# Kernel tuning notes

Hardware: AMD Instinct MI355X
Metric: run time of the kernel (lower is better)

## Reference

```python
import jax, jax.numpy as jnp
import numpy as np

EMBED_DIM = 1024
NUM_HEADS = 16
HEAD_DIM = EMBED_DIM // NUM_HEADS


def setup_inputs() -> dict:
    key = jax.random.key(0)
    ks = jax.random.split(key, 10)
    s = 1.0 / np.sqrt(EMBED_DIM)
    inp = {
        "x1": jax.random.normal(ks[0], (4, 1024, EMBED_DIM), jnp.float32),
        "x2": jax.random.normal(ks[1], (4, 2048, EMBED_DIM), jnp.float32),
        "Wq": jax.random.normal(ks[2], (EMBED_DIM, EMBED_DIM), jnp.float32) * s,
        "bq": jnp.zeros((EMBED_DIM,), jnp.float32),
        "Wk": jax.random.normal(ks[3], (EMBED_DIM, EMBED_DIM), jnp.float32) * s,
        "bk": jnp.zeros((EMBED_DIM,), jnp.float32),
        "Wv": jax.random.normal(ks[4], (EMBED_DIM, EMBED_DIM), jnp.float32) * s,
        "bv": jnp.zeros((EMBED_DIM,), jnp.float32),
        "Wo": jax.random.normal(ks[5], (EMBED_DIM, EMBED_DIM), jnp.float32) * s,
        "bo": jnp.zeros((EMBED_DIM,), jnp.float32),
    }
    return inp


def reference(x1, x2, Wq, bq, Wk, bk, Wv, bv, Wo, bo):
    B, Sq, E = x1.shape
    Skv = x2.shape[1]
    H, D = NUM_HEADS, HEAD_DIM
    # linear projections (PyTorch Linear: x @ W.T + b)
    q = (x1 @ Wq.T + bq).reshape(B, Sq, H, D).transpose(0, 2, 1, 3)   # [B,H,Sq,D]
    k = (x2 @ Wk.T + bk).reshape(B, Skv, H, D).transpose(0, 2, 1, 3)  # [B,H,Skv,D]
    v = (x2 @ Wv.T + bv).reshape(B, Skv, H, D).transpose(0, 2, 1, 3)
    scores = jnp.einsum("bhqd,bhkd->bhqk", q, k) / jnp.sqrt(jnp.float32(D))
    attn = jax.nn.softmax(scores, axis=-1)
    out = jnp.einsum("bhqk,bhkd->bhqd", attn, v)
    out = out.transpose(0, 2, 1, 3).reshape(B, Sq, E)
    return out @ Wo.T + bo
```

## Files before the change

kernel.cpp:

```cpp
#include <hip/hip_runtime.h>

typedef __attribute__((ext_vector_type(8))) short short8;
typedef __attribute__((ext_vector_type(4))) short short4v;
typedef __attribute__((ext_vector_type(4))) float f32x4;
typedef _Float16 half8 __attribute__((ext_vector_type(8)));

#define ASYNC16(g, l) __builtin_amdgcn_global_load_lds( \
    (__attribute__((address_space(1))) void*)(g), \
    (__attribute__((address_space(3))) void*)(l), 16, 0, 0)

__device__ __forceinline__ short f2bf(float f) {
  union { float f; unsigned u; } v; v.f = f;
  unsigned r = v.u + 0x7fffu + ((v.u >> 16) & 1u);
  return (short)(r >> 16);
}

__device__ __forceinline__ short f2h(float f) {
  _Float16 h = (_Float16)f;
  return __builtin_bit_cast(short, h);
}

__device__ __forceinline__ unsigned pkh2(float a, float b) {
  return __builtin_bit_cast(unsigned, __builtin_amdgcn_cvt_pkrtz(a, b));
}

__device__ __forceinline__ f32x4 fzero4() {
  f32x4 z; z[0] = 0.f; z[1] = 0.f; z[2] = 0.f; z[3] = 0.f; return z;
}

__device__ __forceinline__ void wg_barrier() {
  asm volatile("s_waitcnt lgkmcnt(0)\n\ts_barrier" ::: "memory");
}

__device__ __forceinline__ void wait4_barrier() {
  asm volatile("s_waitcnt vmcnt(4)\n\ts_barrier" ::: "memory");
}
__device__ __forceinline__ void wait6_barrier() {
  asm volatile("s_waitcnt vmcnt(6)\n\ts_barrier" ::: "memory");
}
__device__ __forceinline__ void wait0_barrier() {
  asm volatile("s_waitcnt vmcnt(0)\n\ts_barrier" ::: "memory");
}

__global__ __launch_bounds__(256) void cvt_all(
    const float* __restrict__ x1, const float* __restrict__ x2,
    const float* __restrict__ wq, const float* __restrict__ wk,
    const float* __restrict__ wv, const float* __restrict__ wo,
    short* __restrict__ dst) {
  long e = ((long)blockIdx.x * 256 + threadIdx.x) * 4;
  const float* src; long loc;
  if (e < 4194304L)       { src = x1; loc = e; }
  else if (e < 12582912L) { src = x2; loc = e - 4194304L; }
  else if (e < 13631488L) { src = wq; loc = e - 12582912L; }
  else if (e < 14680064L) { src = wk; loc = e - 13631488L; }
  else if (e < 15728640L) { src = wv; loc = e - 14680064L; }
  else                    { src = wo; loc = e - 15728640L; }
  float4 v = *(const float4*)(src + loc);
  short4v o;
  o[0] = f2bf(v.x); o[1] = f2bf(v.y); o[2] = f2bf(v.z); o[3] = f2bf(v.w);
  *(short4v*)(dst + e) = o;
}

__global__ __launch_bounds__(256) void proj(
    const short* __restrict__ xb1, const short* __restrict__ xb2,
    const short* __restrict__ wqp, const short* __restrict__ wkp, const short* __restrict__ wvp,
    const float* __restrict__ bq, const float* __restrict__ bk, const float* __restrict__ bv,
    short* __restrict__ qb, short* __restrict__ kb, short* __restrict__ vb) {
  __shared__ short smem[16384];
  const int tid = threadIdx.x, w = tid >> 6, lane = tid & 63;
  const int quad = lane >> 4, col = lane & 15;
  const int waveM = (w >> 1) * 64, waveN = (w & 1) * 64;
  const int my = blockIdx.x, bn = blockIdx.y * 128;
  const short* A; const short* W; const float* bias; int mode, bm;
  if (my < 32)      { A = xb1; W = wqp; bias = bq; mode = 0; bm = my * 128; }
  else if (my < 96) { A = xb2; W = wkp; bias = bk; mode = 1; bm = (my - 32) * 128; }
  else              { A = xb2; W = wvp; bias = bv; mode = 2; bm = (my - 96) * 128; }

  f32x4 acc[4][4];
  for (int mi = 0; mi < 4; ++mi)
    for (int ni = 0; ni < 4; ++ni)
      acc[mi][ni] = fzero4();

  const int srow = w * 16 + (lane >> 2), scol = (lane & 3) * 8;
  const short* ga = A + (size_t)(bm + srow) * 1024 + scol;
  const short* gb = W + (size_t)(bn + srow) * 1024 + scol;

  auto stage = [&](int b, int kk) {
    short* lA = smem + b * 8192 + w * 512;
    short* lB = smem + b * 8192 + 4096 + w * 512;
    ASYNC16(ga + kk,         lA);
    ASYNC16(ga + kk + 65536, lA + 2048);
    ASYNC16(gb + kk,         lB);
    ASYNC16(gb + kk + 65536, lB + 2048);
  };
  auto compute = [&](int b) {
    const short* As_ = smem + b * 8192;
    const short* Bs_ = As_ + 4096;
    short8 af[4], bf[4];
    for (int mi = 0; mi < 4; ++mi)
      af[mi] = *(const short8*)(As_ + (waveM + mi * 16 + col) * 32 + quad * 8);
    for (int ni = 0; ni < 4; ++ni)
      bf[ni] = *(const short8*)(Bs_ + (waveN + ni * 16 + col) * 32 + quad * 8);
    for (int mi = 0; mi < 4; ++mi)
      for (int ni = 0; ni < 4; ++ni)
        acc[mi][ni] = __builtin_amdgcn_mfma_f32_16x16x32_bf16(af[mi], bf[ni], acc[mi][ni], 0, 0, 0);
  };

  stage(0, 0);
  stage(1, 32);
  for (int it = 0; it < 30; ++it) {
    wait4_barrier();
    compute(it & 1);
    wg_barrier();
    stage(it & 1, (it + 2) * 32);
  }
  wait4_barrier();
  compute(0);
  wait0_barrier();
  compute(1);

  for (int ni = 0; ni < 4; ++ni) {
    int nn = waveN + ni * 16 + col;
    float bvl = bias[bn + nn];
    for (int mi = 0; mi < 4; ++mi) {
      int m0 = waveM + mi * 16 + quad * 4;
      for (int r = 0; r < 4; ++r) {
        int m = m0 + r;
        float val = acc[mi][ni][r] + bvl;
        short sv;
        if (mode == 0)      sv = f2bf(val * 0.18033688011112042f);
        else if (mode == 1) sv = f2bf(val);
        else                sv = f2h(val);
        smem[m * 128 + (nn ^ ((m & 15) << 3))] = sv;
      }
    }
  }
  __syncthreads();
  if (mode < 2) {
    const int S = (mode == 0) ? 1024 : 2048;
    short* outp = (mode == 0) ? qb : kb;
    const int bb = bm / S, s0 = bm & (S - 1), h0 = bn >> 6;
    for (int it = 0; it < 8; ++it) {
      int f = (it * 256 + tid) * 8;
      int hh = f >> 13, rem = f & 8191, m = rem >> 6, d = rem & 63;
      int nn = hh * 64 + d;
      short8 val = *(const short8*)&smem[m * 128 + (nn ^ ((m & 15) << 3))];
      *(short8*)(outp + ((((size_t)(bb * 16 + h0 + hh)) * S + s0 + m) * 64 + d)) = val;
    }
  } else {
    const int bb = bm >> 11, s0 = bm & 2047, kt0 = s0 >> 6, h0 = bn >> 6;
    for (int it = 0; it < 8; ++it) {
      int f = (it * 256 + tid) * 8;
      int hh = f >> 13, rem = f & 8191, ktl = rem >> 12, r3 = rem & 4095;
      int d = r3 >> 6, kvp0 = r3 & 63;
      int nn = hh * 64 + d;
      short8 val;
      for (int j = 0; j < 8; ++j) {
        int kvp = kvp0 + j;
        int kv = ((kvp & 3) << 4) | (kvp >> 2);
        int m = ktl * 64 + kv;
        val[j] = smem[m * 128 + (nn ^ ((m & 15) << 3))];
      }
      *(short8*)(vb + ((((size_t)(bb * 16 + h0 + hh)) * 32 + (kt0 + ktl)) * 4096) + d * 64 + kvp0) = val;
    }
  }
}

__global__ __launch_bounds__(256) void out_gemm(
    const short* __restrict__ A, const short* __restrict__ W,
    const float* __restrict__ bias, float* __restrict__ out) {
  __shared__ short smem[24576];
  const int tid = threadIdx.x, w = tid >> 6, lane = tid & 63;
  const int quad = lane >> 4, col = lane & 15;
  const int waveM = (w >> 1) * 64, waveN = (w & 1) * 32;
  const int bn = blockIdx.x * 64, bm = blockIdx.y * 128;

  f32x4 acc[4][2];
  for (int mi = 0; mi < 4; ++mi)
    for (int ni = 0; ni < 2; ++ni)
      acc[mi][ni] = fzero4();

  const int arow = w * 16 + (lane >> 2), ac = (lane & 3) * 8;
  const short* ga = A + (size_t)(bm + arow) * 1024 + ac;
  const short* gb = W + (size_t)(bn + (tid >> 2)) * 1024 + (tid & 3) * 8;

  auto stage = [&](int b, int kk) {
    short* base = smem + b * 12288;
    short* lA0 = base + w * 512;
    short* lA1 = base + 4096 + w * 512;
    short* lB0 = base + 8192 + w * 512;
    short* lB1 = base + 10240 + w * 512;
    ASYNC16(ga + kk,              lA0);
    ASYNC16(ga + kk + 65536,      lA0 + 2048);
    ASYNC16(ga + kk + 32,         lA1);
    ASYNC16(ga + kk + 32 + 65536, lA1 + 2048);
    ASYNC16(gb + kk,              lB0);
    ASYNC16(gb + kk + 32,         lB1);
  };
  auto compute = [&](int b) {
    const short* base = smem + b * 12288;
    for (int kh = 0; kh < 2; ++kh) {
      const short* Ash = base + kh * 4096;
      const short* Bsh = base + 8192 + kh * 2048;
      short8 af[4], bf[2];
      for (int mi = 0; mi < 4; ++mi)
        af[mi] = *(const short8*)(Ash + (waveM + mi * 16 + col) * 32 + quad * 8);
      for (int ni = 0; ni < 2; ++ni)
        bf[ni] = *(const short8*)(Bsh + (waveN + ni * 16 + col) * 32 + quad * 8);
      for (int mi = 0; mi < 4; ++mi)
        for (int ni = 0; ni < 2; ++ni)
          acc[mi][ni] = __builtin_amdgcn_mfma_f32_16x16x32_bf16(af[mi], bf[ni], acc[mi][ni], 0, 0, 0);
    }
  };

  stage(0, 0);
  stage(1, 64);
  for (int it = 0; it < 14; ++it) {
    wait6_barrier();
    compute(it & 1);
    wg_barrier();
    stage(it & 1, (it + 2) * 64);
  }
  wait6_barrier();
  compute(0);
  wait0_barrier();
  compute(1);

  for (int ni = 0; ni < 2; ++ni) {
    int n = bn + waveN + ni * 16 + col;
    float bvl = bias[n];
    for (int mi = 0; mi < 4; ++mi) {
      int m0 = bm + waveM + mi * 16 + quad * 4;
      for (int r = 0; r < 4; ++r)
        out[(size_t)(m0 + r) * 1024 + n] = acc[mi][ni][r] + bvl;
    }
  }
}

__global__ __launch_bounds__(256, 2) void attn(
    const short* __restrict__ Q, const short* __restrict__ K,
    const short* __restrict__ V, short* __restrict__ O) {
  __shared__ short Ks[128 * 72];
  __shared__ short Vs[80 * 136];
  __shared__ short Ps[128 * 136];
  const int tid = threadIdx.x, w = tid >> 6, lane = tid & 63;
  const int quad = lane >> 4, col = lane & 15;
  const int bh = blockIdx.x, qt = blockIdx.y;
  const int b = bh >> 4, h = bh & 15;
  const int qbase = w * 32;

  const short* qp = Q + ((size_t)bh * 1024 + qt * 128) * 64;
  const short* kp = K + (size_t)bh * 131072;
  const short* vp = V + (size_t)bh * 131072;

  short8 aq[2][2];
  for (int mi = 0; mi < 2; ++mi) {
    const short* qr = qp + (qbase + mi * 16 + col) * 64 + quad * 8;
    aq[mi][0] = *(const short8*)qr;
    aq[mi][1] = *(const short8*)(qr + 32);
  }

  f32x4 oa[2][5];
  for (int mi = 0; mi < 2; ++mi)
    for (int ni = 0; ni < 5; ++ni)
      oa[mi][ni] = fzero4();

  for (int i = tid; i < 16 * 136; i += 256)
    Vs[64 * 136 + i] = (i < 136) ? (short)0x3C00 : (short)0;

  const int krow = lane + (w >> 1) * 64, kch = (w & 1) * 32;
  const int vd = lane, vch = w & 1, vkh = (w >> 1) * 32;

  short8 kpre[4], vpre[4];
  {
    const short* kg = kp + krow * 64 + kch;
    const short* vg = vp + vch * 4096 + vd * 64 + vkh;
    for (int i = 0; i < 4; ++i) kpre[i] = *(const short8*)(kg + i * 8);
    for (int i = 0; i < 4; ++i) vpre[i] = *(const short8*)(vg + i * 8);
  }

  for (int kt = 0; kt < 16; ++kt) {
    wg_barrier();
    for (int i = 0; i < 4; ++i)
      *(short8*)&Ks[krow * 72 + kch + i * 8] = kpre[i];
    for (int i = 0; i < 4; ++i)
      *(short8*)&Vs[vd * 136 + vch * 64 + vkh + i * 8] = vpre[i];
    {
      int ktn = (kt < 15) ? kt + 1 : kt;
      const short* kg = kp + ktn * 8192 + krow * 64 + kch;
      const short* vg = vp + (2 * ktn + vch) * 4096 + vd * 64 + vkh;
      for (int i = 0; i < 4; ++i) kpre[i] = *(const short8*)(kg + i * 8);
      for (int i = 0; i < 4; ++i) vpre[i] = *(const short8*)(vg + i * 8);
    }
    wg_barrier();

    f32x4 sf[2][8];
    for (int nk = 0; nk < 8; ++nk) {
      short8 bk0 = *(const short8*)&Ks[(nk * 16 + col) * 72 + quad * 8];
      short8 bk1 = *(const short8*)&Ks[(nk * 16 + col) * 72 + 32 + quad * 8];
      f32x4 z0 = fzero4(), z1 = fzero4();
      z0 = __builtin_amdgcn_mfma_f32_16x16x32_bf16(aq[0][0], bk0, z0, 0, 0, 0);
      z0 = __builtin_amdgcn_mfma_f32_16x16x32_bf16(aq[0][1], bk1, z0, 0, 0, 0);
      z1 = __builtin_amdgcn_mfma_f32_16x16x32_bf16(aq[1][0], bk0, z1, 0, 0, 0);
      z1 = __builtin_amdgcn_mfma_f32_16x16x32_bf16(aq[1][1], bk1, z1, 0, 0, 0);
      sf[0][nk] = z0;
      sf[1][nk] = z1;
    }

    for (int mi = 0; mi < 2; ++mi)
      for (int nk = 0; nk < 8; ++nk)
        for (int r = 0; r < 4; ++r)
          sf[mi][nk][r] = __builtin_amdgcn_exp2f(sf[mi][nk][r]);
    for (int mi = 0; mi < 2; ++mi)
      for (int r = 0; r < 4; ++r) {
        int row = qbase + mi * 16 + quad * 4 + r;
        uint2 d0, d1;
        d0.x = pkh2(sf[mi][0][r], sf[mi][1][r]);
        d0.y = pkh2(sf[mi][2][r], sf[mi][3][r]);
        d1.x = pkh2(sf[mi][4][r], sf[mi][5][r]);
        d1.y = pkh2(sf[mi][6][r], sf[mi][7][r]);
        *(uint2*)&Ps[row * 136 + col * 4]      = d0;
        *(uint2*)&Ps[row * 136 + 64 + col * 4] = d1;
      }

    for (int ks = 0; ks < 4; ++ks) {
      int koff = ks * 32 + quad * 8;
      half8 ap0 = *(const half8*)&Ps[(qbase + col) * 136 + koff];
      half8 ap1 = *(const half8*)&Ps[(qbase + 16 + col) * 136 + koff];
      for (int ni = 0; ni < 5; ++ni) {
        half8 bv = *(const half8*)&Vs[(ni * 16 + col) * 136 + koff];
        oa[0][ni] = __builtin_amdgcn_mfma_f32_16x16x32_f16(ap0, bv, oa[0][ni], 0, 0, 0);
        oa[1][ni] = __builtin_amdgcn_mfma_f32_16x16x32_f16(ap1, bv, oa[1][ni], 0, 0, 0);
      }
    }
  }

  float inv[2][4];
  for (int mi = 0; mi < 2; ++mi)
    for (int r = 0; r < 4; ++r) {
      float s = __shfl(oa[mi][4][r], lane & 48);
      inv[mi][r] = 1.f / s;
    }
  __syncthreads();
  for (int mi = 0; mi < 2; ++mi)
    for (int ni = 0; ni < 4; ++ni)
      for (int r = 0; r < 4; ++r)
        Ps[(qbase + mi * 16 + quad * 4 + r) * 64 + ni * 16 + col] = f2bf(oa[mi][ni][r] * inv[mi][r]);
  __syncthreads();
  for (int it = 0; it < 4; ++it) {
    int f = (it * 256 + tid) * 8;
    int q = f >> 6, d = f & 63;
    short8 val = *(const short8*)&Ps[q * 64 + d];
    *(short8*)(O + ((size_t)(b * 1024 + qt * 128 + q)) * 1024 + h * 64 + d) = val;
  }
}

extern "C" void kernel_launch(void* const* d_in, const int* in_sizes, int n_in,
                              void* d_out, int out_size, void* d_ws, size_t ws_size,
                              hipStream_t stream) {
  const float* x1 = (const float*)d_in[0];
  const float* x2 = (const float*)d_in[1];
  const float* Wq = (const float*)d_in[2];
  const float* bq = (const float*)d_in[3];
  const float* Wk = (const float*)d_in[4];
  const float* bk = (const float*)d_in[5];
  const float* Wv = (const float*)d_in[6];
  const float* bv = (const float*)d_in[7];
  const float* Wo = (const float*)d_in[8];
  const float* bo = (const float*)d_in[9];

  char* ws = (char*)d_ws;
  short* xb1 = (short*)(ws + 0);
  short* xb2 = (short*)(ws + 8388608);
  short* wqb = (short*)(ws + 25165824);
  short* wkb = (short*)(ws + 27262976);
  short* wvb = (short*)(ws + 29360128);
  short* wob = (short*)(ws + 31457280);
  short* qb  = (short*)(ws + 33554432);
  short* kb  = (short*)(ws + 41943040);
  short* vb  = (short*)(ws + 58720256);
  short* ob  = (short*)(ws + 75497472);

  cvt_all<<<16384, 256, 0, stream>>>(x1, x2, Wq, Wk, Wv, Wo, (short*)ws);
  proj<<<dim3(160, 8), 256, 0, stream>>>(xb1, xb2, wqb, wkb, wvb, bq, bk, bv, qb, kb, vb);
  attn<<<dim3(64, 8), 256, 0, stream>>>(qb, kb, vb, ob);
  out_gemm<<<dim3(16, 32), 256, 0, stream>>>(ob, wob, bo, (float*)d_out);
}
```

Baseline: 233.9 us.

## Replace double-buffered projection loop with single-buffer sync loop; add MFMA priority hints

The projection GEMM drops its two-stage async LDS double buffering with vmcnt-based waits and uses a plain single-buffered loop with __syncthreads before and after each stage. Separately, the attention kernel raises wave priority with s_setprio around the QK^T and PV MFMA blocks. The simpler projection loop removes load/compute overlap and exposes global-load latency, while the priority hints aim to favour matrix work when several waves compete for the unit.

```diff
diff --git a/kernel.cpp b/kernel.cpp
--- a/kernel.cpp
+++ b/kernel.cpp
@@ -32,9 +32,6 @@
   asm volatile("s_waitcnt lgkmcnt(0)\n\ts_barrier" ::: "memory");
 }
 
-__device__ __forceinline__ void wait4_barrier() {
-  asm volatile("s_waitcnt vmcnt(4)\n\ts_barrier" ::: "memory");
-}
 __device__ __forceinline__ void wait6_barrier() {
   asm volatile("s_waitcnt vmcnt(6)\n\ts_barrier" ::: "memory");
 }
@@ -67,6 +64,8 @@
     const float* __restrict__ bq, const float* __restrict__ bk, const float* __restrict__ bv,
     short* __restrict__ qb, short* __restrict__ kb, short* __restrict__ vb) {
   __shared__ short smem[16384];
+  short* As = smem;
+  short* Bs = smem + 4096;
   const int tid = threadIdx.x, w = tid >> 6, lane = tid & 63;
   const int quad = lane >> 4, col = lane & 15;
   const int waveM = (w >> 1) * 64, waveN = (w & 1) * 64;
@@ -84,41 +83,27 @@
   const int srow = w * 16 + (lane >> 2), scol = (lane & 3) * 8;
   const short* ga = A + (size_t)(bm + srow) * 1024 + scol;
   const short* gb = W + (size_t)(bn + srow) * 1024 + scol;
-
-  auto stage = [&](int b, int kk) {
-    short* lA = smem + b * 8192 + w * 512;
-    short* lB = smem + b * 8192 + 4096 + w * 512;
+  short* lA = As + w * 512;
+  short* lB = Bs + w * 512;
+
+  for (int kk = 0; kk < 1024; kk += 32) {
+    __syncthreads();
     ASYNC16(ga + kk,         lA);
     ASYNC16(ga + kk + 65536, lA + 2048);
     ASYNC16(gb + kk,         lB);
     ASYNC16(gb + kk + 65536, lB + 2048);
-  };
-  auto compute = [&](int b) {
-    const short* As_ = smem + b * 8192;
-    const short* Bs_ = As_ + 4096;
+    __syncthreads();
     short8 af[4], bf[4];
     for (int mi = 0; mi < 4; ++mi)
-      af[mi] = *(const short8*)(As_ + (waveM + mi * 16 + col) * 32 + quad * 8);
+      af[mi] = *(const short8*)(As + (waveM + mi * 16 + col) * 32 + quad * 8);
     for (int ni = 0; ni < 4; ++ni)
-      bf[ni] = *(const short8*)(Bs_ + (waveN + ni * 16 + col) * 32 + quad * 8);
+      bf[ni] = *(const short8*)(Bs + (waveN + ni * 16 + col) * 32 + quad * 8);
     for (int mi = 0; mi < 4; ++mi)
       for (int ni = 0; ni < 4; ++ni)
         acc[mi][ni] = __builtin_amdgcn_mfma_f32_16x16x32_bf16(af[mi], bf[ni], acc[mi][ni], 0, 0, 0);
-  };
-
-  stage(0, 0);
-  stage(1, 32);
-  for (int it = 0; it < 30; ++it) {
-    wait4_barrier();
-    compute(it & 1);
-    wg_barrier();
-    stage(it & 1, (it + 2) * 32);
-  }
-  wait4_barrier();
-  compute(0);
-  wait0_barrier();
-  compute(1);
-
+  }
+
+  __syncthreads();
   for (int ni = 0; ni < 4; ++ni) {
     int nn = waveN + ni * 16 + col;
     float bvl = bias[bn + nn];
@@ -295,6 +280,7 @@
     wg_barrier();
 
     f32x4 sf[2][8];
+    __builtin_amdgcn_s_setprio(1);
     for (int nk = 0; nk < 8; ++nk) {
       short8 bk0 = *(const short8*)&Ks[(nk * 16 + col) * 72 + quad * 8];
       short8 bk1 = *(const short8*)&Ks[(nk * 16 + col) * 72 + 32 + quad * 8];
@@ -306,6 +292,7 @@
       sf[0][nk] = z0;
       sf[1][nk] = z1;
     }
+    __builtin_amdgcn_s_setprio(0);
 
     for (int mi = 0; mi < 2; ++mi)
       for (int nk = 0; nk < 8; ++nk)
@@ -323,6 +310,7 @@
         *(uint2*)&Ps[row * 136 + 64 + col * 4] = d1;
       }
 
+    __builtin_amdgcn_s_setprio(1);
     for (int ks = 0; ks < 4; ++ks) {
       int koff = ks * 32 + quad * 8;
       half8 ap0 = *(const half8*)&Ps[(qbase + col) * 136 + koff];
@@ -333,6 +321,7 @@
         oa[1][ni] = __builtin_amdgcn_mfma_f32_16x16x32_f16(ap1, bv, oa[1][ni], 0, 0, 0);
       }
     }
+    __builtin_amdgcn_s_setprio(0);
   }
 
   float inv[2][4];
```

Measured after the change: 236.7 us. Within noise of the previous version (+1.2%).
